# Optimization experiments

Measured on AMD Instinct MI355X. Metric: run time of the kernel, lower is better.

Reference implementation:

```python
import jax, jax.numpy as jnp
import numpy as np

G, B, T, D, U = 3, 32, 1024, 512, 512  # branches, batch, time, feat dim, units

def setup_inputs() -> dict:
    key = jax.random.key(0)
    ks = jax.random.split(key, 8)
    s = 0.02
    return {
        "query": jax.random.normal(ks[0], (G, B, D), jnp.float32),
        "values": jax.random.normal(ks[1], (G, B, T, D), jnp.float32),
        "W1": jax.random.normal(ks[2], (G, D, U), jnp.float32) * s,
        "b1": jnp.zeros((G, U), jnp.float32),
        "W2": jax.random.normal(ks[3], (G, D, U), jnp.float32) * s,
        "b2": jnp.zeros((G, U), jnp.float32),
        "V": jax.random.normal(ks[4], (G, U), jnp.float32) * s,
        "bV": jnp.zeros((G,), jnp.float32),
    }

def reference(query, values, W1, b1, W2, b2, V, bV):
    # query: [G,B,D], values: [G,B,T,D]; G=3 independent additive-attention branches.
    qp = jnp.einsum('gbd,gdu->gbu', query, W1) + b1[:, None, :]          # [G,B,U]
    vp = jnp.einsum('gbtd,gdu->gbtu', values, W2) + b2[:, None, None, :]  # [G,B,T,U]
    feat = jnp.tanh(qp[:, :, None, :] + vp)                               # [G,B,T,U]
    score = jnp.einsum('gbtu,gu->gbt', feat, V) + bV[:, None, None]       # [G,B,T]
    weights = jax.nn.softmax(score, axis=2)                               # softmax over time
    context = jnp.einsum('gbt,gbtd->gbd', weights, values)                # [G,B,D]
    return context, weights[..., None]  # matches tf.stack outputs: [3,B,D], [3,B,T,1]
```

## Files before the change

kernel.cpp:

```cpp
#include <hip/hip_runtime.h>
#include <cstdint>
#include <cstddef>

#define NG 3
#define NB 32
#define NT 1024
#define ND 512
#define NU 512

typedef __bf16 bf16x8 __attribute__((ext_vector_type(8)));
typedef float  f32x16 __attribute__((ext_vector_type(16)));

static __device__ __forceinline__ unsigned int f2bf(float f) {
    union { float f; unsigned int u; } v; v.f = f;
    return (v.u + 0x7FFFu + ((v.u >> 16) & 1u)) >> 16;
}

static __device__ __forceinline__ unsigned int cvt_pk_bf16(float lo, float hi) {
    unsigned int r;
    asm("v_cvt_pk_bf16_f32 %0, %1, %2" : "=v"(r) : "v"(lo), "v"(hi));
    return r;
}

static __device__ __forceinline__ bf16x8 ld_bf16x8(const char* base, int off) {
    return __builtin_bit_cast(bf16x8, *(const uint4*)(base + off));
}

#define AS1(p) ((const __attribute__((address_space(1))) void*)(p))
#define AS3(p) ((__attribute__((address_space(3))) void*)(p))

__global__ __launch_bounds__(256) void prep_qb_kernel(
    const float* __restrict__ query, const float* __restrict__ W1,
    const float* __restrict__ b1, const float* __restrict__ b2,
    float* __restrict__ qb)
{
    __shared__ float qs[NB][ND];
    const int g  = blockIdx.x >> 3;
    const int uc = blockIdx.x & 7;
    const int tid = threadIdx.x;

    const float4* qsrc = (const float4*)(query + (size_t)g * NB * ND);
    #pragma unroll
    for (int i = 0; i < 16; ++i)
        ((float4*)&qs[0][0])[tid + i * 256] = qsrc[tid + i * 256];
    __syncthreads();

    const int u  = uc * 64 + (tid & 63);
    const int b0 = tid >> 6;
    float acc[8] = {};
    const float* w1col = W1 + (size_t)g * ND * NU + u;
    for (int d = 0; d < ND; ++d) {
        float w = w1col[(size_t)d * NU];
        #pragma unroll
        for (int j = 0; j < 8; ++j)
            acc[j] = fmaf(qs[b0 + 4 * j][d], w, acc[j]);
    }
    const float bias = b1[g * NU + u] + b2[g * NU + u];
    #pragma unroll
    for (int j = 0; j < 8; ++j)
        qb[((size_t)g * NB + (b0 + 4 * j)) * NU + u] = acc[j] + bias;
}

__global__ __launch_bounds__(256) void prep_w2t_kernel(
    const float* __restrict__ W2, char* __restrict__ w2t)
{
    __shared__ float tile[64][65];
    const int g  = blockIdx.x >> 6;
    const int tb = blockIdx.x & 63;
    const int d0 = (tb >> 3) * 64;
    const int u0 = (tb & 7) * 64;
    const int tx = threadIdx.x & 63;
    const int ty = threadIdx.x >> 6;

    const float* src = W2 + (size_t)g * ND * NU;
    #pragma unroll
    for (int k = 0; k < 16; ++k) {
        int r = ty + 4 * k;
        tile[r][tx] = src[(size_t)(d0 + r) * NU + (u0 + tx)];
    }
    __syncthreads();
    char* dstg = w2t + (size_t)g * 16 * 32768;
    #pragma unroll
    for (int k = 0; k < 16; ++k) {
        int ul = ty + 4 * k;
        int u  = u0 + ul;
        int d  = d0 + tx;
        unsigned short h = (unsigned short)f2bf(tile[tx][ul]);
        int r = u & 31;
        size_t off = (size_t)(u >> 5) * 32768
                   + (size_t)(((r << 10) | (d << 1)) ^ ((r & 7) << 4));
        *(unsigned short*)(dstg + off) = h;
    }
}

__global__ __launch_bounds__(256) void score_kernel(
    const float* __restrict__ values, const char* __restrict__ w2t,
    const float* __restrict__ qb, const float* __restrict__ Vvec,
    const float* __restrict__ bV, float* __restrict__ scores)
{
    __shared__ char  Bs[3][16384];
    __shared__ float qbs[NU];
    __shared__ float Vs[NU];

    const int blk = blockIdx.x;
    const int g   = blk >> 8;
    const int rem = blk & 255;
    const int b   = rem >> 3;
    const int t0  = (rem & 7) << 7;
    const int tid  = threadIdx.x;
    const int lane = tid & 63;
    const int wave = tid >> 6;

    const char* w2g = w2t + ((size_t)g << 19);

    auto stage = [&](int ph, char* buf) {
        const char* src = w2g + ((size_t)(ph >> 1) << 15) + ((ph & 1) << 9)
                        + (wave << 13) + ((lane >> 5) << 10) + ((lane & 31) << 4);
        char* dst = buf + (wave << 12) + (lane << 4);
        #pragma unroll
        for (int i = 0; i < 4; ++i)
            __builtin_amdgcn_global_load_lds(AS1(src + (i << 11)),
                                             AS3(dst + (i << 10)), 16, 0, 0);
    };

    {
        const float* qsrc = qb + ((size_t)g * NB + b) * NU;
        const float* vsrc = Vvec + (size_t)g * NU;
        __builtin_amdgcn_global_load_lds(AS1(qsrc + tid),       AS3(&qbs[tid]),       4, 0, 0);
        __builtin_amdgcn_global_load_lds(AS1(qsrc + tid + 256), AS3(&qbs[tid + 256]), 4, 0, 0);
        __builtin_amdgcn_global_load_lds(AS1(vsrc + tid),       AS3(&Vs[tid]),        4, 0, 0);
        __builtin_amdgcn_global_load_lds(AS1(vsrc + tid + 256), AS3(&Vs[tid + 256]),  4, 0, 0);
    }
    stage(0, Bs[0]);
    stage(1, Bs[1]);

    bf16x8 afrag[32];
    {
        const int arow_t = t0 + (wave << 5) + (lane & 31);
        const float* arow = values + (((size_t)g * NB + b) * NT + arow_t) * ND;
        const int acol = (lane >> 5) << 3;
        #pragma unroll
        for (int kk = 0; kk < 32; ++kk) {
            const float4* ap = (const float4*)(arow + (kk << 4) + acol);
            float4 v0 = ap[0], v1 = ap[1];
            union { bf16x8 v; unsigned int u[4]; } t;
            t.u[0] = cvt_pk_bf16(v0.x, v0.y);
            t.u[1] = cvt_pk_bf16(v0.z, v0.w);
            t.u[2] = cvt_pk_bf16(v1.x, v1.y);
            t.u[3] = cvt_pk_bf16(v1.z, v1.w);
            afrag[kk] = t.v;
        }
    }

    asm volatile("s_waitcnt vmcnt(0) lgkmcnt(0)" ::: "memory");
    __builtin_amdgcn_s_barrier();

    const int brow  = lane & 31;
    const int bswz  = (brow & 7) << 4;
    const int bbase = (brow << 9) + ((lane >> 5) << 4);

    float p[16] = {};

    char* bA = (char*)Bs[0];
    char* bB = (char*)Bs[1];
    char* bC = (char*)Bs[2];

    #pragma unroll 1
    for (int uc = 0; uc < 16; ++uc) {
        const int ph0 = uc << 1;
        f32x16 acc0 = (f32x16)(0.0f);
        f32x16 acc1 = (f32x16)(0.0f);

        if (uc < 15) stage(ph0 + 2, bC);
        __builtin_amdgcn_s_setprio(1);
        #pragma unroll
        for (int kk = 0; kk < 16; kk += 2) {
            bf16x8 b0 = ld_bf16x8(bA, (bbase + (kk << 5)) ^ bswz);
            bf16x8 b1 = ld_bf16x8(bA, (bbase + ((kk + 1) << 5)) ^ bswz);
            acc0 = __builtin_amdgcn_mfma_f32_32x32x16_bf16(afrag[kk],     b0, acc0, 0, 0, 0);
            acc1 = __builtin_amdgcn_mfma_f32_32x32x16_bf16(afrag[kk + 1], b1, acc1, 0, 0, 0);
        }
        __builtin_amdgcn_s_setprio(0);
        if (uc < 15) {
            asm volatile("s_waitcnt vmcnt(4)" ::: "memory");
        } else {
            asm volatile("s_waitcnt vmcnt(0)" ::: "memory");
        }
        __builtin_amdgcn_s_barrier();

        if (uc < 15) stage(ph0 + 3, bA);
        __builtin_amdgcn_s_setprio(1);
        #pragma unroll
        for (int kk = 0; kk < 16; kk += 2) {
            bf16x8 b0 = ld_bf16x8(bB, (bbase + (kk << 5)) ^ bswz);
            bf16x8 b1 = ld_bf16x8(bB, (bbase + ((kk + 1) << 5)) ^ bswz);
            acc0 = __builtin_amdgcn_mfma_f32_32x32x16_bf16(afrag[16 + kk],     b0, acc0, 0, 0, 0);
            acc1 = __builtin_amdgcn_mfma_f32_32x32x16_bf16(afrag[16 + kk + 1], b1, acc1, 0, 0, 0);
        }
        __builtin_amdgcn_s_setprio(0);

        {
            const int u = (uc << 5) + brow;
            const float qv = qbs[u], vv = Vs[u];
            #pragma unroll
            for (int r = 0; r < 16; ++r) {
                float x  = (acc0[r] + acc1[r]) + qv;
                float e  = exp2f(2.8853900817779268f * x);
                float th = 1.0f - 2.0f * __builtin_amdgcn_rcpf(e + 1.0f);
                p[r] = fmaf(th, vv, p[r]);
            }
        }

        if (uc < 15) {
            asm volatile("s_waitcnt vmcnt(4)" ::: "memory");
            __builtin_amdgcn_s_barrier();
        }

        char* t = bA; bA = bC; bC = bB; bB = t;
    }

    #pragma unroll
    for (int r = 0; r < 16; ++r) {
        float v = p[r];
        v += __shfl_xor(v, 1);
        v += __shfl_xor(v, 2);
        v += __shfl_xor(v, 4);
        v += __shfl_xor(v, 8);
        v += __shfl_xor(v, 16);
        p[r] = v;
    }
    if ((lane & 31) == 0) {
        const float bv = bV[g];
        float* srow = scores + ((size_t)g * NB + b) * NT + t0 + (wave << 5);
        #pragma unroll
        for (int r = 0; r < 16; ++r) {
            int t_local = (r & 3) + 8 * (r >> 2) + 4 * (lane >> 5);
            srow[t_local] = p[r] + bv;
        }
    }
}

__global__ __launch_bounds__(256) void finish_kernel(
    const float* __restrict__ scores, const float* __restrict__ values,
    float* __restrict__ out_ctx, float* __restrict__ out_w)
{
    __shared__ float sl[NT];
    __shared__ float red[16];
    __shared__ float cred[4][128];
    const int blk   = blockIdx.x;
    const int gb    = blk >> 2;
    const int slice = blk & 3;
    const int tid = threadIdx.x;
    const int lane = tid & 63, wid = tid >> 6;

    const float* srow = scores + (size_t)gb * NT;
    float s[4];
    #pragma unroll
    for (int j = 0; j < 4; ++j) s[j] = srow[tid + 256 * j];

    float m = fmaxf(fmaxf(s[0], s[1]), fmaxf(s[2], s[3]));
    #pragma unroll
    for (int mask = 32; mask; mask >>= 1) m = fmaxf(m, __shfl_xor(m, mask));
    if (lane == 0) red[wid] = m;
    __syncthreads();
    const float gm = fmaxf(fmaxf(red[0], red[1]), fmaxf(red[2], red[3]));

    float e[4], ps = 0.f;
    #pragma unroll
    for (int j = 0; j < 4; ++j) { e[j] = __expf(s[j] - gm); ps += e[j]; }
    #pragma unroll
    for (int mask = 32; mask; mask >>= 1) ps += __shfl_xor(ps, mask);
    if (lane == 0) red[8 + wid] = ps;
    __syncthreads();
    const float inv = 1.f / (red[8] + red[9] + red[10] + red[11]);

    #pragma unroll
    for (int j = 0; j < 4; ++j) {
        float w = e[j] * inv;
        sl[tid + 256 * j] = w;
        if (slice == 0) out_w[(size_t)gb * NT + tid + 256 * j] = w;
    }
    __syncthreads();

    const int dp = tid & 63;
    const int tg = tid >> 6;
    const float* vbase = values + (size_t)gb * NT * ND + slice * 128 + dp * 2;
    float ax = 0.f, ay = 0.f;
    #pragma unroll 4
    for (int t = tg; t < NT; t += 4) {
        float2 v = *(const float2*)(vbase + (size_t)t * ND);
        float w = sl[t];
        ax = fmaf(w, v.x, ax);
        ay = fmaf(w, v.y, ay);
    }
    cred[tg][dp * 2]     = ax;
    cred[tg][dp * 2 + 1] = ay;
    __syncthreads();
    if (tid < 128) {
        float r = cred[0][tid] + cred[1][tid] + cred[2][tid] + cred[3][tid];
        out_ctx[(size_t)gb * ND + slice * 128 + tid] = r;
    }
}

extern "C" void kernel_launch(void* const* d_in, const int* in_sizes, int n_in,
                              void* d_out, int out_size, void* d_ws, size_t ws_size,
                              hipStream_t stream)
{
    (void)in_sizes; (void)n_in; (void)out_size; (void)ws_size;
    const float* query  = (const float*)d_in[0];
    const float* values = (const float*)d_in[1];
    const float* W1     = (const float*)d_in[2];
    const float* b1     = (const float*)d_in[3];
    const float* W2     = (const float*)d_in[4];
    const float* b2     = (const float*)d_in[5];
    const float* Vv     = (const float*)d_in[6];
    const float* bV     = (const float*)d_in[7];

    float* out_ctx = (float*)d_out;
    float* out_w   = out_ctx + (size_t)NG * NB * ND;

    float* qb     = (float*)d_ws;
    float* scores = qb + (size_t)NG * NB * NU;
    char*  w2t    = (char*)(scores + (size_t)NG * NB * NT);

    prep_qb_kernel <<<NG * 8,             256, 0, stream>>>(query, W1, b1, b2, qb);
    prep_w2t_kernel<<<NG * 64,            256, 0, stream>>>(W2, w2t);
    score_kernel   <<<NG * NB * (NT/128), 256, 0, stream>>>(values, w2t, qb, Vv, bV, scores);
    finish_kernel  <<<NG * NB * 4,        256, 0, stream>>>(scores, values, out_ctx, out_w);
}
```

Baseline: 175.3 us.

## Retile score GEMM to 256x256 blocks with K-streamed A/B double buffering

Restructures the score kernel so each 512-thread block computes a 256(time)x256(unit) tile, streaming both the bf16-converted values and the W2 image through double-buffered LDS along the K dimension. Before, each 128-row block held the full-K values fragment in registers and swept all 512 units. The larger tile raises MFMA arithmetic intensity per LDS byte and splits the U dimension across two blocks. Their partial scores are written separately and summed, together with bV, in the finish kernel. The cost is more LDS (about 130KB per block), which limits occupancy, plus an extra partial-score buffer and a cross-wave reduction through shared memory.

```diff
diff --git a/kernel.cpp b/kernel.cpp
--- a/kernel.cpp
+++ b/kernel.cpp
@@ -79,169 +79,192 @@
         tile[r][tx] = src[(size_t)(d0 + r) * NU + (u0 + tx)];
     }
     __syncthreads();
-    char* dstg = w2t + (size_t)g * 16 * 32768;
     #pragma unroll
     for (int k = 0; k < 16; ++k) {
         int ul = ty + 4 * k;
         int u  = u0 + ul;
         int d  = d0 + tx;
         unsigned short h = (unsigned short)f2bf(tile[tx][ul]);
-        int r = u & 31;
-        size_t off = (size_t)(u >> 5) * 32768
-                   + (size_t)(((r << 10) | (d << 1)) ^ ((r & 7) << 4));
-        *(unsigned short*)(dstg + off) = h;
-    }
-}
-
-__global__ __launch_bounds__(256) void score_kernel(
+        int nb2 = u >> 8, up = u & 255, ksd = d >> 6, kp = d & 63;
+        size_t off = ((size_t)((((g << 1) + nb2) << 3) + ksd) << 15)
+                   + (size_t)((up << 7) + (((kp << 1) ^ ((up & 7) << 4))));
+        *(unsigned short*)(w2t + off) = h;
+    }
+}
+
+__global__ __launch_bounds__(512, 2) void score_kernel(
     const float* __restrict__ values, const char* __restrict__ w2t,
-    const float* __restrict__ qb, const float* __restrict__ Vvec,
-    const float* __restrict__ bV, float* __restrict__ scores)
-{
-    __shared__ char  Bs[3][16384];
-    __shared__ float qbs[NU];
-    __shared__ float Vs[NU];
-
-    const int blk = blockIdx.x;
-    const int g   = blk >> 8;
-    const int rem = blk & 255;
-    const int b   = rem >> 3;
-    const int t0  = (rem & 7) << 7;
+    const float* __restrict__ qbg, const float* __restrict__ Vvec,
+    float* __restrict__ part0, float* __restrict__ part1)
+{
+    __shared__ char Abuf[2][32768];
+    __shared__ char Bbuf[2][32768];
+    __shared__ float qbs[256];
+    __shared__ float Vs[256];
+    __shared__ float spart[4][256];
+
+    const int blk  = blockIdx.x;
+    const int g    = blk >> 8;
+    const int rr   = blk & 255;
+    const int mt   = rr >> 1;
+    const int nb   = rr & 1;
+    const int b    = mt >> 2;
+    const int t0   = (mt & 3) << 8;
     const int tid  = threadIdx.x;
     const int lane = tid & 63;
     const int wave = tid >> 6;
-
-    const char* w2g = w2t + ((size_t)g << 19);
-
-    auto stage = [&](int ph, char* buf) {
-        const char* src = w2g + ((size_t)(ph >> 1) << 15) + ((ph & 1) << 9)
-                        + (wave << 13) + ((lane >> 5) << 10) + ((lane & 31) << 4);
-        char* dst = buf + (wave << 12) + (lane << 4);
+    const int wm   = wave >> 2;
+    const int wn   = wave & 3;
+    const int rl   = lane & 31;
+    const int hi   = lane >> 5;
+
+    const char* bimg = w2t + ((size_t)((((g << 1) + nb) << 3)) << 15);
+
+    if (wave < 4) {
+        const float* qsrc = qbg + (((size_t)(g * NB + b)) << 9) + (nb << 8) + (wave << 6) + lane;
+        __builtin_amdgcn_global_load_lds(AS1(qsrc), AS3(&qbs[(wave << 6) + lane]), 4, 0, 0);
+    } else {
+        const float* vsrc = Vvec + (g << 9) + (nb << 8) + ((wave - 4) << 6) + lane;
+        __builtin_amdgcn_global_load_lds(AS1(vsrc), AS3(&Vs[((wave - 4) << 6) + lane]), 4, 0, 0);
+    }
+
+    auto stageB = [&](int ks, char* dst) {
+        const char* src = bimg + ((size_t)ks << 15) + (wave << 12) + (lane << 4);
+        char* d = dst + (wave << 12) + (lane << 4);
         #pragma unroll
         for (int i = 0; i < 4; ++i)
-            __builtin_amdgcn_global_load_lds(AS1(src + (i << 11)),
-                                             AS3(dst + (i << 10)), 16, 0, 0);
+            __builtin_amdgcn_global_load_lds(AS1(src + (i << 10)), AS3(d + (i << 10)), 16, 0, 0);
     };
 
-    {
-        const float* qsrc = qb + ((size_t)g * NB + b) * NU;
-        const float* vsrc = Vvec + (size_t)g * NU;
-        __builtin_amdgcn_global_load_lds(AS1(qsrc + tid),       AS3(&qbs[tid]),       4, 0, 0);
-        __builtin_amdgcn_global_load_lds(AS1(qsrc + tid + 256), AS3(&qbs[tid + 256]), 4, 0, 0);
-        __builtin_amdgcn_global_load_lds(AS1(vsrc + tid),       AS3(&Vs[tid]),        4, 0, 0);
-        __builtin_amdgcn_global_load_lds(AS1(vsrc + tid + 256), AS3(&Vs[tid + 256]),  4, 0, 0);
-    }
-    stage(0, Bs[0]);
-    stage(1, Bs[1]);
-
-    bf16x8 afrag[32];
-    {
-        const int arow_t = t0 + (wave << 5) + (lane & 31);
-        const float* arow = values + (((size_t)g * NB + b) * NT + arow_t) * ND;
-        const int acol = (lane >> 5) << 3;
-        #pragma unroll
-        for (int kk = 0; kk < 32; ++kk) {
-            const float4* ap = (const float4*)(arow + (kk << 4) + acol);
-            float4 v0 = ap[0], v1 = ap[1];
-            union { bf16x8 v; unsigned int u[4]; } t;
-            t.u[0] = cvt_pk_bf16(v0.x, v0.y);
-            t.u[1] = cvt_pk_bf16(v0.z, v0.w);
-            t.u[2] = cvt_pk_bf16(v1.x, v1.y);
-            t.u[3] = cvt_pk_bf16(v1.z, v1.w);
-            afrag[kk] = t.v;
-        }
-    }
-
+    const int arow  = tid >> 1;
+    const int ahalf = tid & 1;
+    const float* aptr = values
+        + (((size_t)((g * NB + b) * NT + t0 + arow)) << 9) + (ahalf << 5);
+    const int awswz = (arow & 7) << 4;
+
+    float4 av[8];
+    auto loadA = [&](int ks) {
+        const float4* p4 = (const float4*)(aptr + (ks << 6));
+        #pragma unroll
+        for (int i = 0; i < 8; ++i) av[i] = p4[i];
+    };
+    auto writeA = [&](char* dst) {
+        char* base = dst + (arow << 7);
+        #pragma unroll
+        for (int q = 0; q < 4; ++q) {
+            uint4 w;
+            w.x = cvt_pk_bf16(av[2*q].x,   av[2*q].y);
+            w.y = cvt_pk_bf16(av[2*q].z,   av[2*q].w);
+            w.z = cvt_pk_bf16(av[2*q+1].x, av[2*q+1].y);
+            w.w = cvt_pk_bf16(av[2*q+1].z, av[2*q+1].w);
+            *(uint4*)(base + (((ahalf << 6) + (q << 4)) ^ awswz)) = w;
+        }
+    };
+
+    const int lswz = (rl & 7) << 4;
+    int koff[4];
+    #pragma unroll
+    for (int kf = 0; kf < 4; ++kf) koff[kf] = ((kf << 5) + (hi << 4)) ^ lswz;
+    const int abase = (((wm << 7) + rl) << 7);
+    const int bbase = (((wn << 6) + rl) << 7);
+
+    f32x16 acc[4][2];
+    #pragma unroll
+    for (int mf = 0; mf < 4; ++mf) {
+        acc[mf][0] = (f32x16)(0.0f);
+        acc[mf][1] = (f32x16)(0.0f);
+    }
+
+    char* Ac = Abuf[0]; char* An = Abuf[1];
+    char* Bc = Bbuf[0]; char* Bn = Bbuf[1];
+
+    stageB(0, Bc);
+    loadA(0);
     asm volatile("s_waitcnt vmcnt(0) lgkmcnt(0)" ::: "memory");
+    writeA(Ac);
+    asm volatile("s_waitcnt lgkmcnt(0)" ::: "memory");
     __builtin_amdgcn_s_barrier();
 
-    const int brow  = lane & 31;
-    const int bswz  = (brow & 7) << 4;
-    const int bbase = (brow << 9) + ((lane >> 5) << 4);
-
-    float p[16] = {};
-
-    char* bA = (char*)Bs[0];
-    char* bB = (char*)Bs[1];
-    char* bC = (char*)Bs[2];
-
     #pragma unroll 1
-    for (int uc = 0; uc < 16; ++uc) {
-        const int ph0 = uc << 1;
-        f32x16 acc0 = (f32x16)(0.0f);
-        f32x16 acc1 = (f32x16)(0.0f);
-
-        if (uc < 15) stage(ph0 + 2, bC);
+    for (int ks = 0; ks < 8; ++ks) {
+        if (ks < 7) {
+            stageB(ks + 1, Bn);
+            loadA(ks + 1);
+        }
         __builtin_amdgcn_s_setprio(1);
         #pragma unroll
-        for (int kk = 0; kk < 16; kk += 2) {
-            bf16x8 b0 = ld_bf16x8(bA, (bbase + (kk << 5)) ^ bswz);
-            bf16x8 b1 = ld_bf16x8(bA, (bbase + ((kk + 1) << 5)) ^ bswz);
-            acc0 = __builtin_amdgcn_mfma_f32_32x32x16_bf16(afrag[kk],     b0, acc0, 0, 0, 0);
-            acc1 = __builtin_amdgcn_mfma_f32_32x32x16_bf16(afrag[kk + 1], b1, acc1, 0, 0, 0);
+        for (int kf = 0; kf < 4; ++kf) {
+            bf16x8 a0 = ld_bf16x8(Ac, abase         + koff[kf]);
+            bf16x8 a1 = ld_bf16x8(Ac, abase +  4096 + koff[kf]);
+            bf16x8 a2 = ld_bf16x8(Ac, abase +  8192 + koff[kf]);
+            bf16x8 a3 = ld_bf16x8(Ac, abase + 12288 + koff[kf]);
+            bf16x8 b0 = ld_bf16x8(Bc, bbase         + koff[kf]);
+            bf16x8 b1 = ld_bf16x8(Bc, bbase +  4096 + koff[kf]);
+            acc[0][0] = __builtin_amdgcn_mfma_f32_32x32x16_bf16(a0, b0, acc[0][0], 0, 0, 0);
+            acc[0][1] = __builtin_amdgcn_mfma_f32_32x32x16_bf16(a0, b1, acc[0][1], 0, 0, 0);
+            acc[1][0] = __builtin_amdgcn_mfma_f32_32x32x16_bf16(a1, b0, acc[1][0], 0, 0, 0);
+            acc[1][1] = __builtin_amdgcn_mfma_f32_32x32x16_bf16(a1, b1, acc[1][1], 0, 0, 0);
+            acc[2][0] = __builtin_amdgcn_mfma_f32_32x32x16_bf16(a2, b0, acc[2][0], 0, 0, 0);
+            acc[2][1] = __builtin_amdgcn_mfma_f32_32x32x16_bf16(a2, b1, acc[2][1], 0, 0, 0);
+            acc[3][0] = __builtin_amdgcn_mfma_f32_32x32x16_bf16(a3, b0, acc[3][0], 0, 0, 0);
+            acc[3][1] = __builtin_amdgcn_mfma_f32_32x32x16_bf16(a3, b1, acc[3][1], 0, 0, 0);
         }
         __builtin_amdgcn_s_setprio(0);
-        if (uc < 15) {
-            asm volatile("s_waitcnt vmcnt(4)" ::: "memory");
-        } else {
+        if (ks < 7) {
             asm volatile("s_waitcnt vmcnt(0)" ::: "memory");
-        }
-        __builtin_amdgcn_s_barrier();
-
-        if (uc < 15) stage(ph0 + 3, bA);
-        __builtin_amdgcn_s_setprio(1);
-        #pragma unroll
-        for (int kk = 0; kk < 16; kk += 2) {
-            bf16x8 b0 = ld_bf16x8(bB, (bbase + (kk << 5)) ^ bswz);
-            bf16x8 b1 = ld_bf16x8(bB, (bbase + ((kk + 1) << 5)) ^ bswz);
-            acc0 = __builtin_amdgcn_mfma_f32_32x32x16_bf16(afrag[16 + kk],     b0, acc0, 0, 0, 0);
-            acc1 = __builtin_amdgcn_mfma_f32_32x32x16_bf16(afrag[16 + kk + 1], b1, acc1, 0, 0, 0);
-        }
-        __builtin_amdgcn_s_setprio(0);
-
-        {
-            const int u = (uc << 5) + brow;
-            const float qv = qbs[u], vv = Vs[u];
+            writeA(An);
+            asm volatile("s_waitcnt lgkmcnt(0)" ::: "memory");
+            __builtin_amdgcn_s_barrier();
+            char* t1 = Ac; Ac = An; An = t1;
+            char* t2 = Bc; Bc = Bn; Bn = t2;
+        }
+    }
+
+    const float qv0 = qbs[(wn << 6) + rl];
+    const float qv1 = qbs[(wn << 6) + 32 + rl];
+    const float vv0 = Vs[(wn << 6) + rl];
+    const float vv1 = Vs[(wn << 6) + 32 + rl];
+    const float CL = 2.8853900817779268f;
+    #pragma unroll
+    for (int mf = 0; mf < 4; ++mf) {
+        float p[16];
+        #pragma unroll
+        for (int r2 = 0; r2 < 16; ++r2) {
+            float x0 = acc[mf][0][r2] + qv0;
+            float x1 = acc[mf][1][r2] + qv1;
+            float e0 = exp2f(CL * x0);
+            float e1 = exp2f(CL * x1);
+            float th0 = 1.f - 2.f * __builtin_amdgcn_rcpf(e0 + 1.f);
+            float th1 = 1.f - 2.f * __builtin_amdgcn_rcpf(e1 + 1.f);
+            p[r2] = fmaf(th1, vv1, th0 * vv0);
+        }
+        #pragma unroll
+        for (int r2 = 0; r2 < 16; ++r2) {
+            float v = p[r2];
+            v += __shfl_xor(v, 1);
+            v += __shfl_xor(v, 2);
+            v += __shfl_xor(v, 4);
+            v += __shfl_xor(v, 8);
+            v += __shfl_xor(v, 16);
+            p[r2] = v;
+        }
+        if (rl == 0) {
             #pragma unroll
-            for (int r = 0; r < 16; ++r) {
-                float x  = (acc0[r] + acc1[r]) + qv;
-                float e  = exp2f(2.8853900817779268f * x);
-                float th = 1.0f - 2.0f * __builtin_amdgcn_rcpf(e + 1.0f);
-                p[r] = fmaf(th, vv, p[r]);
-            }
-        }
-
-        if (uc < 15) {
-            asm volatile("s_waitcnt vmcnt(4)" ::: "memory");
-            __builtin_amdgcn_s_barrier();
-        }
-
-        char* t = bA; bA = bC; bC = bB; bB = t;
-    }
-
-    #pragma unroll
-    for (int r = 0; r < 16; ++r) {
-        float v = p[r];
-        v += __shfl_xor(v, 1);
-        v += __shfl_xor(v, 2);
-        v += __shfl_xor(v, 4);
-        v += __shfl_xor(v, 8);
-        v += __shfl_xor(v, 16);
-        p[r] = v;
-    }
-    if ((lane & 31) == 0) {
-        const float bv = bV[g];
-        float* srow = scores + ((size_t)g * NB + b) * NT + t0 + (wave << 5);
-        #pragma unroll
-        for (int r = 0; r < 16; ++r) {
-            int t_local = (r & 3) + 8 * (r >> 2) + 4 * (lane >> 5);
-            srow[t_local] = p[r] + bv;
-        }
+            for (int r2 = 0; r2 < 16; ++r2)
+                spart[wn][(wm << 7) + (mf << 5) + (r2 & 3) + 8 * (r2 >> 2) + 4 * hi] = p[r2];
+        }
+    }
+    __syncthreads();
+    if (tid < 256) {
+        float s = spart[0][tid] + spart[1][tid] + spart[2][tid] + spart[3][tid];
+        float* dst = nb ? part1 : part0;
+        dst[(((size_t)(g * NB + b)) << 10) + t0 + tid] = s;
     }
 }
 
 __global__ __launch_bounds__(256) void finish_kernel(
-    const float* __restrict__ scores, const float* __restrict__ values,
+    const float* __restrict__ part0, const float* __restrict__ part1,
+    const float* __restrict__ bV, const float* __restrict__ values,
     float* __restrict__ out_ctx, float* __restrict__ out_w)
 {
     __shared__ float sl[NT];
@@ -252,11 +275,14 @@
     const int slice = blk & 3;
     const int tid = threadIdx.x;
     const int lane = tid & 63, wid = tid >> 6;
-
-    const float* srow = scores + (size_t)gb * NT;
+    const float bv = bV[gb >> 5];
+
     float s[4];
     #pragma unroll
-    for (int j = 0; j < 4; ++j) s[j] = srow[tid + 256 * j];
+    for (int j = 0; j < 4; ++j) {
+        int idx = (int)((size_t)gb * NT) + tid + 256 * j;
+        s[j] = part0[idx] + part1[idx] + bv;
+    }
 
     float m = fmaxf(fmaxf(s[0], s[1]), fmaxf(s[2], s[3]));
     #pragma unroll
@@ -319,12 +345,13 @@
     float* out_ctx = (float*)d_out;
     float* out_w   = out_ctx + (size_t)NG * NB * ND;
 
-    float* qb     = (float*)d_ws;
-    float* scores = qb + (size_t)NG * NB * NU;
-    char*  w2t    = (char*)(scores + (size_t)NG * NB * NT);
-
-    prep_qb_kernel <<<NG * 8,             256, 0, stream>>>(query, W1, b1, b2, qb);
-    prep_w2t_kernel<<<NG * 64,            256, 0, stream>>>(W2, w2t);
-    score_kernel   <<<NG * NB * (NT/128), 256, 0, stream>>>(values, w2t, qb, Vv, bV, scores);
-    finish_kernel  <<<NG * NB * 4,        256, 0, stream>>>(scores, values, out_ctx, out_w);
-}
+    float* qb    = (float*)d_ws;
+    float* part0 = qb + (size_t)NG * NB * NU;
+    float* part1 = part0 + (size_t)NG * NB * NT;
+    char*  w2t   = (char*)(part1 + (size_t)NG * NB * NT);
+
+    prep_qb_kernel <<<NG * 8,   256, 0, stream>>>(query, W1, b1, b2, qb);
+    prep_w2t_kernel<<<NG * 64,  256, 0, stream>>>(W2, w2t);
+    score_kernel   <<<NG * 256, 512, 0, stream>>>(values, w2t, qb, Vv, part0, part1);
+    finish_kernel  <<<NG * NB * 4, 256, 0, stream>>>(part0, part1, bV, values, out_ctx, out_w);
+}
```

After: 177.7 us. About the same (+1.4%).
